# Kernel optimization log

Hardware: AMD Instinct MI355X
Metric: run time of the kernel (lower is better)

## Reference

```python
import jax, jax.numpy as jnp
import numpy as np

N, E, IN_DIM, OUT_DIM, NNZ = 4096, 2048, 256, 256, 65536
ALPHA = 0.2          # LeakyReLU negative slope
NEG_GAT = -9e15      # masked_fill value for GAT adjacency mask
NEG_ATT = -1e9       # masked_fill value inside ScaledDotProductAttention_hyper


def setup_inputs() -> dict:
    key = jax.random.key(0)
    ks = jax.random.split(key, 10)
    stdv = 1.0 / np.sqrt(OUT_DIM)
    u = lambda k, shape: jax.random.uniform(k, shape, jnp.float32, -stdv, stdv)
    x = jax.random.normal(ks[0], (N, IN_DIM), jnp.float32)
    node_idx = jax.random.randint(ks[1], (NNZ,), 0, N, jnp.int32)
    edge_idx = jax.random.randint(ks[2], (NNZ,), 0, E, jnp.int32)
    hyperedge_index = jnp.stack([node_idx, edge_idx])  # [2, NNZ]
    return {
        "x": x,
        "weight": u(ks[3], (IN_DIM, OUT_DIM)),
        "weight2": u(ks[4], (IN_DIM, OUT_DIM)),
        "weight3": u(ks[5], (OUT_DIM, OUT_DIM)),
        "weight_g": u(ks[6], (IN_DIM, OUT_DIM)),
        "a_g": u(ks[7], (2 * OUT_DIM, 1)),
        "word_context": u(ks[8], (1, OUT_DIM)),
        "bias": u(ks[9], (OUT_DIM,)),
        "hyperedge_index": hyperedge_index,
        "num_edges": E,
    }


def reference(x, weight, weight2, weight3, weight_g, a_g, word_context, bias,
              hyperedge_index, num_edges):
    n = x.shape[0]
    d = weight_g.shape[1]
    temp = d ** 0.5  # temperature = out_features ** 0.5

    # --- hypergraph preprocessing: dense incidence H [N, E] and node adjacency A [N, N]
    H = jnp.zeros((n, num_edges), x.dtype).at[hyperedge_index[0], hyperedge_index[1]].set(1.0)
    A = (H @ H.T > 0).astype(x.dtype)
    A = A.at[jnp.arange(n), jnp.arange(n)].set(1.0)  # fill_diagonal_(1)

    # --- dense GAT-style attention over the clique-expanded graph
    Wh_g = x @ weight_g                               # [N, D]
    Wh1 = Wh_g @ a_g[:d]                              # [N, 1]
    Wh2 = Wh_g @ a_g[d:]                              # [N, 1]
    e_g = jax.nn.leaky_relu(Wh1 + Wh2.T, ALPHA)       # [N, N]
    attention_g = jax.nn.softmax(jnp.where(A > 0, e_g, NEG_GAT), axis=1)

    # --- project node-node attention onto hyperedges: [N, E]
    graph2hyper = attention_g @ H

    # --- dual hypergraph cross-attention (eval mode: dropout is identity)
    x_4att = x @ weight2                              # [N, D]
    xw = x @ weight + bias                            # [N, D] (transfer=True)

    # attention1: hyperedge queries attend over nodes, mask = H.T [E, N]
    q1 = jnp.broadcast_to(word_context[0], (num_edges, d))
    attn1 = (q1 / temp) @ x_4att.T                    # [E, N]
    attn1 = jnp.where(H.T == 0, NEG_ATT, attn1)
    att1 = jax.nn.softmax(graph2hyper.T, axis=-1) + jax.nn.softmax(attn1, axis=-1)
    edge = att1 @ xw                                  # [E, D]
    att2he = att1.T                                   # [N, E]

    # attention2: node queries attend over hyperedges, mask = H [N, E]
    edge_4att = edge @ weight3                        # [E, D]
    attn2 = (x_4att / temp) @ edge_4att.T             # [N, E]
    attn2 = jnp.where(H == 0, NEG_ATT, attn2)
    att2hn = jax.nn.softmax(graph2hyper, axis=-1) + jax.nn.softmax(attn2, axis=-1)
    node = att2hn @ edge                              # [N, D]

    # --- combine attentions and aggregate
    att2_he_out = att2he @ att2he.T                   # [N, N]
    att2_hn_out = att2hn @ att2hn.T                   # [N, N]
    attention_out = attention_g + att2_he_out + att2_hn_out
    h_prime_g = jax.nn.elu(attention_out @ Wh_g)      # concat=True -> ELU

    node = jax.nn.relu(node)                          # concat=True -> ReLU, then squeeze
    return node, h_prime_g
```

## Files before the change

kernel.cpp:

```cpp
#include <hip/hip_runtime.h>
#include <cstdint>
#include <cstddef>


#define DI __device__ __forceinline__
typedef unsigned short u16;
typedef unsigned int   u32;
typedef __bf16 bf16x8 __attribute__((ext_vector_type(8)));
typedef float  f32x4  __attribute__((ext_vector_type(4)));
typedef u32    u32x4  __attribute__((ext_vector_type(4)));

constexpr int NN  = 4096;
constexpr int EE  = 2048;
constexpr int NNZb = 65536;

constexpr size_t MB = (size_t)1 << 20;
constexpr size_t OFF_HBITS   = 0;
constexpr size_t OFF_HBITST  = 1*MB;
constexpr size_t OFF_ABITS   = 2*MB;
constexpr size_t OFF_EDGE    = 2*MB;
constexpr size_t OFF_WH1     = 4*MB;
constexpr size_t OFF_WH2     = 4*MB + 16384;
constexpr size_t OFF_V       = 4*MB + 32768;
constexpr size_t OFF_RSINV   = 4*MB + 49152;
constexpr size_t OFF_WCAT    = 5*MB;
constexpr size_t OFF_XB      = 6*MB;
constexpr size_t OFF_EDGET   = 6*MB;
constexpr size_t OFF_HN2T    = 7*MB;
constexpr size_t OFF_WHG     = 8*MB;
constexpr size_t OFF_X4ATT   = 10*MB;
constexpr size_t OFF_YB      = 12*MB;
constexpr size_t OFF_XWT     = 14*MB;
constexpr size_t OFF_WHGTA   = 16*MB;
constexpr size_t OFF_HBT     = 18*MB;
constexpr size_t OFF_EDGE2T  = 18*MB;
constexpr size_t OFF_WHGTB   = 34*MB;
constexpr size_t OFF_EXPA    = 36*MB;
constexpr size_t OFF_ATT1    = 36*MB;
constexpr size_t OFF_ATT2HN  = 36*MB;
constexpr size_t OFF_ATT1T   = 52*MB;
constexpr size_t OFF_G2H     = 68*MB;
constexpr size_t OFF_G2HT    = 84*MB;
constexpr size_t OFF_ATT2HNT = 84*MB;
constexpr size_t OFF_ATTN2   = 100*MB;
constexpr size_t OFF_G1      = 116*MB;
constexpr size_t OFF_C2      = 120*MB;
constexpr size_t OFF_HN2ACC  = 124*MB;

DI u16 to_bf(float f) {
  union { float f; u32 u; } x; x.f = f;
  u32 r = x.u + 0x7fffu + ((x.u >> 16) & 1u);
  return (u16)(r >> 16);
}
DI float from_bf(u16 h) { union { u32 u; float f; } x; x.u = (u32)h << 16; return x.f; }
DI void store_bf4(u16* p, float a, float b, float c, float d) {
  u32 lo = (u32)to_bf(a) | ((u32)to_bf(b) << 16);
  u32 hi = (u32)to_bf(c) | ((u32)to_bf(d) << 16);
  *(u32*)p = lo; *((u32*)p + 1) = hi;
}

DI float wredf(float v) {
  #pragma unroll
  for (int o = 32; o; o >>= 1) v += __shfl_down(v, o);
  return v;
}
DI int wredi(int v) {
  #pragma unroll
  for (int o = 32; o; o >>= 1) v += __shfl_down(v, o);
  return v;
}

typedef __attribute__((address_space(3))) void lds_void;
typedef __attribute__((address_space(1))) void glb_void;
DI void async_load16(const void* g, void* l) {
  __builtin_amdgcn_global_load_lds((glb_void*)(uintptr_t)g,
                                   (lds_void*)(u32)(uintptr_t)l, 16, 0, 0);
}

template <int BM, int BN, class Epi>
DI void gemm_body(const u16* __restrict__ A, const u16* __restrict__ B,
                  int nb, int K, int k0, int kLen, Epi epi, int tile,
                  u16* As, u16* Bs)
{
  constexpr int BK = 64;
  constexpr int WM = BM / 2, WN = BN / 2;
  constexpr int FM = WM / 16, FN = WN / 16;
  constexpr int AI = (BM * 8) / 256, BI = (BN * 8) / 256;

  const int tid = threadIdx.x;
  const int w = tid >> 6, l = tid & 63;
  const int bi = tile / nb, bj = tile - bi * nb;
  const int i0 = bi * BM, j0 = bj * BN;
  const int wm = (w & 1) * WM, wn = (w >> 1) * WN;
  const int quad = l >> 4, m16 = l & 15;

  f32x4 acc[FM][FN] = {};

  for (int kb = k0; kb < k0 + kLen; kb += BK) {
    __syncthreads();
    #pragma unroll
    for (int i = 0; i < AI; ++i) {
      const int ci = (i * 4 + w) * 64 + l;
      const int r = ci >> 3;
      const int lc = (ci & 7) ^ (r & 7);
      async_load16(A + (size_t)(i0 + r) * K + kb + lc * 8, &As[(i * 4 + w) * 512]);
    }
    #pragma unroll
    for (int i = 0; i < BI; ++i) {
      const int ci = (i * 4 + w) * 64 + l;
      const int r = ci >> 3;
      const int lc = (ci & 7) ^ (r & 7);
      async_load16(B + (size_t)(j0 + r) * K + kb + lc * 8, &Bs[(i * 4 + w) * 512]);
    }
    __syncthreads();
    #pragma unroll
    for (int ks = 0; ks < 2; ++ks) {
      bf16x8 af[FM], bfv[FN];
      #pragma unroll
      for (int mi = 0; mi < FM; ++mi) {
        const int row = wm + mi * 16 + m16;
        af[mi] = *(const bf16x8*)&As[row * BK + (((ks * 4 + quad) ^ (row & 7)) * 8)];
      }
      #pragma unroll
      for (int ni = 0; ni < FN; ++ni) {
        const int row = wn + ni * 16 + m16;
        bfv[ni] = *(const bf16x8*)&Bs[row * BK + (((ks * 4 + quad) ^ (row & 7)) * 8)];
      }
      #pragma unroll
      for (int mi = 0; mi < FM; ++mi)
        #pragma unroll
        for (int ni = 0; ni < FN; ++ni)
          acc[mi][ni] = __builtin_amdgcn_mfma_f32_16x16x32_bf16(
              af[mi], bfv[ni], acc[mi][ni], 0, 0, 0);
    }
  }
  #pragma unroll
  for (int mi = 0; mi < FM; ++mi)
    #pragma unroll
    for (int ni = 0; ni < FN; ++ni) {
      const int rb = i0 + wm + mi * 16 + quad * 4;
      const int c  = j0 + wn + ni * 16 + m16;
      epi(rb, c, acc[mi][ni]);
    }
}

DI void t32_tile(const u16* __restrict__ in, u16* __restrict__ out,
                 int R, int C, int bx, int by, u16* t) {
  int tx = threadIdx.x & 31, ty = threadIdx.x >> 5;
  int x0 = bx * 32, y0 = by * 32;
  #pragma unroll
  for (int k = 0; k < 32; k += 8)
    t[(ty + k) * 33 + tx] = in[(size_t)(y0 + ty + k) * C + x0 + tx];
  __syncthreads();
  #pragma unroll
  for (int k = 0; k < 32; k += 8)
    out[(size_t)(x0 + ty + k) * R + y0 + tx] = t[tx * 33 + ty + k];
}

struct EpiG0 {
  u16 *whg, *whgTa, *whgTb, *x4, *xwT; const float* bias;
  DI void operator()(int r, int c, f32x4 v) const {
    if (c < 256) {
      #pragma unroll
      for (int i = 0; i < 4; ++i) whg[(r + i) * 256 + c] = to_bf(v[i]);
      store_bf4(&whgTa[(size_t)c * NN + r], v[0], v[1], v[2], v[3]);
      store_bf4(&whgTb[(size_t)c * NN + r], v[0], v[1], v[2], v[3]);
    } else if (c < 512) {
      #pragma unroll
      for (int i = 0; i < 4; ++i) x4[(r + i) * 256 + (c - 256)] = to_bf(v[i]);
    } else {
      float b = bias[c - 512];
      store_bf4(&xwT[(size_t)(c - 512) * NN + r], v[0]+b, v[1]+b, v[2]+b, v[3]+b);
    }
  }
};
struct EpiBig {
  const float* rsInv; u16* g2h; u16* g2hT; float* g1;
  DI void operator()(int r, int c, f32x4 v) const {
    float w0 = v[0]*rsInv[r], w1 = v[1]*rsInv[r+1], w2 = v[2]*rsInv[r+2], w3 = v[3]*rsInv[r+3];
    if (c < 2048) {
      g2h[(size_t)r * EE + c] = to_bf(w0);
      g2h[(size_t)(r+1) * EE + c] = to_bf(w1);
      g2h[(size_t)(r+2) * EE + c] = to_bf(w2);
      g2h[(size_t)(r+3) * EE + c] = to_bf(w3);
      store_bf4(&g2hT[(size_t)c * NN + r], w0, w1, w2, w3);
    } else {
      g1[(r) * 256 + (c - 2048)] = w0;
      g1[(r+1) * 256 + (c - 2048)] = w1;
      g1[(r+2) * 256 + (c - 2048)] = w2;
      g1[(r+3) * 256 + (c - 2048)] = w3;
    }
  }
};
struct EpiEdgeT {
  u16 *edgeT, *edge2T, *edge;
  DI void operator()(int r, int c, f32x4 v) const {
    if (r < 256) {
      #pragma unroll
      for (int i = 0; i < 4; ++i) edgeT[(size_t)(r + i) * EE + c] = to_bf(v[i]);
      store_bf4(&edge[(size_t)c * 256 + r], v[0], v[1], v[2], v[3]);
    } else {
      #pragma unroll
      for (int i = 0; i < 4; ++i) edge2T[(size_t)(r - 256 + i) * EE + c] = to_bf(v[i]);
    }
  }
};
struct EpiCombine {
  const float* g1; const float* c2; float* out;
  DI void operator()(int r, int c, f32x4 v) const {
    if (c < 256) {
      #pragma unroll
      for (int i = 0; i < 4; ++i) out[(r + i) * 256 + c] = fmaxf(v[i], 0.f);
    } else {
      int d = c - 256;
      #pragma unroll
      for (int i = 0; i < 4; ++i) {
        float s = g1[(r + i) * 256 + d] + c2[(r + i) * 256 + d] + v[i];
        out[1048576 + (r + i) * 256 + d] = s > 0.f ? s : expm1f(s);
      }
    }
  }
};
struct EpiBf16 { u16* out; int ldn;
  DI void operator()(int r, int c, f32x4 v) const {
    #pragma unroll
    for (int i = 0; i < 4; ++i) out[(size_t)(r + i) * ldn + c] = to_bf(v[i]);
  } };
struct EpiBf16Scale { u16* out; int ldn; float s;
  DI void operator()(int r, int c, f32x4 v) const {
    #pragma unroll
    for (int i = 0; i < 4; ++i) out[(size_t)(r + i) * ldn + c] = to_bf(v[i] * s);
  } };
struct EpiF32 { float* out; int ldn;
  DI void operator()(int r, int c, f32x4 v) const {
    #pragma unroll
    for (int i = 0; i < 4; ++i) out[(size_t)(r + i) * ldn + c] = v[i];
  } };
struct EpiAtomF32 { float* out; int ldn;
  DI void operator()(int r, int c, f32x4 v) const {
    #pragma unroll
    for (int i = 0; i < 4; ++i) atomicAdd(&out[(size_t)(r + i) * ldn + c], v[i]);
  } };

template <int BM, int BN, int S, int LB, int XSW, class Epi>
__global__ __launch_bounds__(256, LB)
void gemm_k(const u16* __restrict__ A, const u16* __restrict__ B,
            int nb, int K, Epi epi) {
  __shared__ __align__(16) u16 smem[(BM + BN) * 64];
  int t = blockIdx.x;
  int k0 = 0, kLen = K;
  if (XSW > 0) {
    const int xcd = t & 7, idx = t >> 3;
    const int bj = xcd * XSW + idx % XSW;
    const int bi = idx / XSW;
    t = bi * nb + bj;
  } else if (S > 1) {
    const int tilesPer = gridDim.x / S;
    const int s = t / tilesPer; t -= s * tilesPer;
    kLen = K / S; k0 = s * kLen;
  }
  gemm_body<BM, BN>(A, B, nb, K, k0, kLen, epi, t, smem, smem + BM * 64);
}

__global__ void k_prep(const float* wg, const float* w2, const float* w1,
                       const float* w3, const float* x, u16* wcat, u16* xb,
                       char* zbits, char* zhbt, char* zhn2) {
  int idx = blockIdx.x * 256 + threadIdx.x;
  if (blockIdx.x < 5120) {
    if (idx < 196608) {
      int blk = idx >> 16, r = idx & 65535;
      int d = r >> 8, kk = r & 255;
      const float* src = blk == 0 ? wg : blk == 1 ? w2 : w1;
      wcat[idx] = to_bf(src[kk * 256 + d]);
    } else if (idx < 262144) {
      int r = idx - 196608;
      wcat[196608 + r] = to_bf(w3[r]);
    } else {
      int r = idx - 262144;
      xb[r] = to_bf(x[r]);
    }
  } else {
    int z = idx - 5120 * 256;
    u32x4 zero = {0, 0, 0, 0};
    if (z < 262144)       ((u32x4*)zbits)[z] = zero;
    else if (z < 1310720) ((u32x4*)zhbt)[z - 262144] = zero;
    else                  ((u32x4*)zhn2)[z - 1310720] = zero;
  }
}

__global__ void k_scatter_diag(const int* __restrict__ hidx, u32* hbits, u32* hbitsT,
                               u16* hbT, u32* abits) {
  int k = blockIdx.x * 256 + threadIdx.x;
  if (k < NNZb) {
    int n = hidx[k], e = hidx[NNZb + k];
    atomicOr(&hbits[n * 64 + (e >> 5)], 1u << (e & 31));
    atomicOr(&hbitsT[e * 128 + (n >> 5)], 1u << (n & 31));
    hbT[(size_t)e * NN + n] = 0x3F80;
  } else {
    int i = k - NNZb;
    if (i < NN) atomicOr(&abits[i * 128 + (i >> 5)], 1u << (i & 31));
  }
}

__global__ void k_rowclique(const u16* __restrict__ whg, const u16* __restrict__ x4,
                            const float* __restrict__ ag, const float* __restrict__ wc,
                            float* wh1, float* wh2, float* v,
                            const u32* __restrict__ hbitsT, u32* abits) {
  __shared__ int list[512];
  __shared__ int cnt;
  int tid = threadIdx.x;
  if (blockIdx.x < 1024) {
    int wv = tid >> 6, l = tid & 63;
    int row = blockIdx.x * 4 + wv;
    float s1 = 0, s2 = 0, s3 = 0;
    #pragma unroll
    for (int dd = 0; dd < 4; ++dd) {
      int d = l * 4 + dd;
      float a = from_bf(whg[row * 256 + d]);
      s1 += a * ag[d]; s2 += a * ag[256 + d];
      s3 += from_bf(x4[row * 256 + d]) * wc[d];
    }
    s1 = wredf(s1); s2 = wredf(s2); s3 = wredf(s3);
    if (l == 0) { wh1[row] = s1; wh2[row] = s2; v[row] = s3 * (1.0f / 16.0f); }
  } else {
    int e = blockIdx.x - 1024;
    if (tid == 0) cnt = 0;
    __syncthreads();
    if (tid < 128) {
      u32 w = hbitsT[e * 128 + tid];
      while (w) {
        int b = __ffs(w) - 1;
        int p = atomicAdd(&cnt, 1);
        if (p < 512) list[p] = tid * 32 + b;
        w &= w - 1;
      }
    }
    __syncthreads();
    int c = cnt < 512 ? cnt : 512;
    for (int p = tid; p < c * c; p += 256) {
      int i = list[p / c], j = list[p % c];
      atomicOr(&abits[i * 128 + (j >> 5)], 1u << (j & 31));
    }
  }
}

__global__ void k_exprows(const u32* __restrict__ abits, const float* __restrict__ wh1,
                          const float* __restrict__ wh2, u16* __restrict__ expA,
                          float* rsInv) {
  int i = blockIdx.x, tid = threadIdx.x;
  __shared__ float w2s[NN];
  __shared__ float ssum;
  for (int j = tid; j < NN; j += 256) w2s[j] = wh2[j];
  if (tid == 0) ssum = 0.f;
  __syncthreads();
  float a = wh1[i], lsum = 0.f;
  for (int j = tid; j < NN; j += 256) {
    u32 w = abits[i * 128 + (j >> 5)];
    u16 h = 0;
    if ((w >> (j & 31)) & 1) {
      float z = a + w2s[j];
      float eg = z > 0.f ? z : 0.2f * z;
      h = to_bf(__expf(eg));
      lsum += from_bf(h);
    }
    expA[(size_t)i * NN + j] = h;
  }
  lsum = wredf(lsum);
  if ((tid & 63) == 0) atomicAdd(&ssum, lsum);
  __syncthreads();
  if (tid == 0) rsInv[i] = 1.0f / ssum;
}

__global__ void k_edge_softmax(const u16* __restrict__ g2hT, const u32* __restrict__ hbitsT,
                               const float* __restrict__ v, u16* __restrict__ att1) {
  int e = blockIdx.x, tid = threadIdx.x;
  __shared__ float evals[NN];
  __shared__ u32 hw[128];
  __shared__ float s1s, s2s; __shared__ int cs;
  if (tid == 0) { s1s = 0.f; s2s = 0.f; cs = 0; }
  if (tid < 128) hw[tid] = hbitsT[e * 128 + tid];
  __syncthreads();
  float sum1 = 0.f;
  for (int j = tid; j < NN; j += 256) {
    float ev = __expf(from_bf(g2hT[(size_t)e * NN + j]));
    evals[j] = ev; sum1 += ev;
  }
  float sum2 = 0.f; int cnt = 0;
  if (tid < 128) {
    u32 w = hw[tid]; cnt = __popc(w);
    while (w) { int b = __ffs(w) - 1; sum2 += __expf(v[tid * 32 + b]); w &= w - 1; }
  }
  sum1 = wredf(sum1); sum2 = wredf(sum2); cnt = wredi(cnt);
  if ((tid & 63) == 0) { atomicAdd(&s1s, sum1); atomicAdd(&s2s, sum2); atomicAdd(&cs, cnt); }
  __syncthreads();
  float inv1 = 1.0f / s1s;
  int c = cs;
  float inv2 = c > 0 ? 1.0f / s2s : 0.0f;
  float unif = c > 0 ? 0.0f : (1.0f / (float)NN);
  for (int j = tid; j < NN; j += 256) {
    float t = evals[j] * inv1 + unif;
    if ((hw[j >> 5] >> (j & 31)) & 1) t += __expf(v[j]) * inv2;
    att1[(size_t)e * NN + j] = to_bf(t);
  }
}

__global__ __launch_bounds__(256, 2)
void k_tri_edge(const u16* __restrict__ Fcat, const u16* __restrict__ Att1,
                EpiEdgeT e0,
                const u16* __restrict__ X4att, const u16* __restrict__ W3b,
                EpiBf16 e1,
                const u16* __restrict__ tin, u16* __restrict__ tout) {
  __shared__ __align__(16) u16 smem[192 * 64];
  int b = blockIdx.x;
  if (b < 256) {
    const int xcd = b & 7, idx = b >> 3;
    const int t = (idx / 4) * 32 + xcd * 4 + (idx & 3);
    gemm_body<64, 64>(Fcat, Att1, 32, NN, 0, NN, e0, t, smem, smem + 64 * 64);
  }
  else if (b < 384) gemm_body<128, 64>(X4att, W3b, 4, 256, 0, 256, e1, b - 256, smem, smem + 128 * 64);
  else { int t = b - 384; t32_tile(tin, tout, EE, NN, t & 127, t >> 7, smem); }
}

__global__ __launch_bounds__(256, 2)
void k_dual_attn2(const u16* __restrict__ Att1T, const u16* __restrict__ Edge2T,
                  EpiF32 e0,
                  const u16* __restrict__ Yb, const u16* __restrict__ Edge,
                  EpiBf16Scale e1) {
  __shared__ __align__(16) u16 smem[256 * 64];
  int b = blockIdx.x;
  if (b < 128) gemm_body<128, 64>(Att1T, Edge2T, 4, EE, 0, EE, e0, b, smem, smem + 128 * 64);
  else         gemm_body<128, 128>(Yb, Edge, 16, 256, 0, 256, e1, b - 128, smem, smem + 128 * 64);
}

__global__ void k_node_softmax(const u16* __restrict__ g2h, const u16* __restrict__ attn2,
                               const u32* __restrict__ hbits, u16* __restrict__ att2hn) {
  int n = blockIdx.x, tid = threadIdx.x;
  __shared__ float ev3[EE], ev4[EE];
  __shared__ u32 hw[64];
  __shared__ float s3s, s4s; __shared__ int cs;
  if (tid == 0) { s3s = 0.f; s4s = 0.f; cs = 0; }
  if (tid < 64) hw[tid] = hbits[n * 64 + tid];
  __syncthreads();
  float s3 = 0.f, s4 = 0.f; int cl = 0;
  for (int e = tid; e < EE; e += 256) {
    float x3 = __expf(from_bf(g2h[(size_t)n * EE + e]));
    ev3[e] = x3; s3 += x3;
    bool m = (hw[e >> 5] >> (e & 31)) & 1;
    float x4 = m ? __expf(from_bf(attn2[(size_t)n * EE + e])) : 0.f;
    ev4[e] = x4; s4 += x4; cl += m;
  }
  s3 = wredf(s3); s4 = wredf(s4); cl = wredi(cl);
  if ((tid & 63) == 0) { atomicAdd(&s3s, s3); atomicAdd(&s4s, s4); atomicAdd(&cs, cl); }
  __syncthreads();
  float inv3 = 1.0f / s3s;
  int c = cs;
  float inv4 = c > 0 ? 1.0f / s4s : 0.0f;
  float unif = c > 0 ? 0.0f : (1.0f / (float)EE);
  for (int e = tid; e < EE; e += 256)
    att2hn[(size_t)n * EE + e] = to_bf(ev3[e] * inv3 + ev4[e] * inv4 + unif);
}

__global__ void k_transpose(const u16* __restrict__ in, u16* __restrict__ out,
                            int R, int C) {
  __shared__ u16 t[32 * 33];
  t32_tile(in, out, R, C, blockIdx.x, blockIdx.y, t);
}

__global__ void k_cast_hn2(const float* __restrict__ acc, u16* __restrict__ hn2T) {
  int idx = blockIdx.x * 256 + threadIdx.x;
  hn2T[idx] = to_bf(acc[idx]);
}

extern "C" void kernel_launch(void* const* d_in, const int* in_sizes, int n_in,
                              void* d_out, int out_size, void* d_ws, size_t ws_size,
                              hipStream_t stream) {
  (void)in_sizes; (void)n_in; (void)out_size; (void)ws_size;
  const float* x    = (const float*)d_in[0];
  const float* w1   = (const float*)d_in[1];
  const float* w2   = (const float*)d_in[2];
  const float* w3   = (const float*)d_in[3];
  const float* wg   = (const float*)d_in[4];
  const float* ag   = (const float*)d_in[5];
  const float* wc   = (const float*)d_in[6];
  const float* bias = (const float*)d_in[7];
  const int*   hidx = (const int*)d_in[8];
  float* out = (float*)d_out;
  char* ws = (char*)d_ws;

  u32* Hbits   = (u32*)(ws + OFF_HBITS);
  u32* HbitsT  = (u32*)(ws + OFF_HBITST);
  u32* Abits   = (u32*)(ws + OFF_ABITS);
  float* Wh1   = (float*)(ws + OFF_WH1);
  float* Wh2   = (float*)(ws + OFF_WH2);
  float* V     = (float*)(ws + OFF_V);
  float* RsInv = (float*)(ws + OFF_RSINV);
  u16* Wcat    = (u16*)(ws + OFF_WCAT);
  u16* W3b     = Wcat + 196608;
  u16* Xb      = (u16*)(ws + OFF_XB);
  u16* Whg     = (u16*)(ws + OFF_WHG);
  u16* X4att   = (u16*)(ws + OFF_X4ATT);
  u16* Yb      = (u16*)(ws + OFF_YB);
  u16* XwT     = (u16*)(ws + OFF_XWT);
  u16* WhgTa   = (u16*)(ws + OFF_WHGTA);
  u16* HbT     = (u16*)(ws + OFF_HBT);
  u16* WhgTb   = (u16*)(ws + OFF_WHGTB);
  u16* ExpA    = (u16*)(ws + OFF_EXPA);
  u16* Att1    = (u16*)(ws + OFF_ATT1);
  u16* Att1T   = (u16*)(ws + OFF_ATT1T);
  u16* Att2hn  = (u16*)(ws + OFF_ATT2HN);
  u16* G2h     = (u16*)(ws + OFF_G2H);
  u16* G2hT    = (u16*)(ws + OFF_G2HT);
  u16* Att2hnT = (u16*)(ws + OFF_ATT2HNT);
  u16* Attn2   = (u16*)(ws + OFF_ATTN2);
  float* G1    = (float*)(ws + OFF_G1);
  float* C2    = (float*)(ws + OFF_C2);
  float* Hn2Acc = (float*)(ws + OFF_HN2ACC);
  u16* Edge    = (u16*)(ws + OFF_EDGE);
  u16* EdgeT   = (u16*)(ws + OFF_EDGET);
  u16* Hn2T    = (u16*)(ws + OFF_HN2T);
  u16* Edge2T  = (u16*)(ws + OFF_EDGE2T);

  k_prep<<<10752, 256, 0, stream>>>(wg, w2, w1, w3, x, Wcat, Xb,
                                    ws + OFF_HBITS, ws + OFF_HBT, ws + OFF_HN2ACC);
  k_scatter_diag<<<272, 256, 0, stream>>>(hidx, Hbits, HbitsT, HbT, Abits);
  gemm_k<128, 64, 1, 3, 0><<<384, 256, 0, stream>>>(
      Xb, Wcat, 12, 256, EpiG0{Whg, WhgTa, WhgTb, X4att, XwT, bias});
  k_rowclique<<<3072, 256, 0, stream>>>(Whg, X4att, ag, wc, Wh1, Wh2, V,
                                        HbitsT, Abits);
  k_exprows<<<NN, 256, 0, stream>>>(Abits, Wh1, Wh2, ExpA, RsInv);
  gemm_k<128, 96, 1, 3, 3><<<768, 256, 0, stream>>>(
      ExpA, HbT, 24, NN, EpiBig{RsInv, G2h, G2hT, G1});
  k_edge_softmax<<<EE, 256, 0, stream>>>(G2hT, HbitsT, V, Att1);
  k_tri_edge<<<8576, 256, 0, stream>>>(
      XwT, Att1, EpiEdgeT{EdgeT, Edge2T, Edge},
      X4att, W3b, EpiBf16{Yb, 256},
      Att1, Att1T);
  k_dual_attn2<<<640, 256, 0, stream>>>(
      Att1T, Edge2T, EpiF32{C2, 256},
      Yb, Edge, EpiBf16Scale{Attn2, EE, 1.0f / 16.0f});
  k_node_softmax<<<NN, 256, 0, stream>>>(G2h, Attn2, Hbits, Att2hn);
  k_transpose<<<dim3(64, 128), 256, 0, stream>>>(Att2hn, Att2hnT, NN, EE);
  gemm_k<64, 64, 4, 3, 0><<<512, 256, 0, stream>>>(
      WhgTa, Att2hnT, 32, NN, EpiAtomF32{Hn2Acc, EE});
  k_cast_hn2<<<2048, 256, 0, stream>>>(Hn2Acc, Hn2T);
  gemm_k<64, 64, 1, 2, 0><<<512, 256, 0, stream>>>(
      Att2hn, EdgeT, 8, EE, EpiCombine{G1, C2, out});
}
```

Before: 380.3 us.

## Run the big exp(A) x [H|Whg] GEMM in FP8 with a dedicated kernel

The large N x N by N x (E+D) GEMM now takes fp8 (e4m3) operands. expA, the incidence matrix H^T and the second transposed copy of Wh_g are stored as fp8, and a new gemm_f8 kernel with swizzled LDS tiles and 16x16x32 fp8 MFMA replaces the bf16 GEMM. This halves the bytes read from memory and the LDS traffic, and doubles MFMA throughput for the largest matmul. In exchange, exp values and Wh_g lose precision, and the XCD tile swizzle of the old GEMM is dropped.

New measurement: 361.4 us. 5.0% less time.

```diff
diff --git a/kernel.cpp b/kernel.cpp
--- a/kernel.cpp
+++ b/kernel.cpp
@@ -5,6 +5,7 @@
 
 #define DI __device__ __forceinline__
 typedef unsigned short u16;
+typedef unsigned char  u8;
 typedef unsigned int   u32;
 typedef __bf16 bf16x8 __attribute__((ext_vector_type(8)));
 typedef float  f32x4  __attribute__((ext_vector_type(4)));
@@ -34,7 +35,7 @@
 constexpr size_t OFF_WHGTA   = 16*MB;
 constexpr size_t OFF_HBT     = 18*MB;
 constexpr size_t OFF_EDGE2T  = 18*MB;
-constexpr size_t OFF_WHGTB   = 34*MB;
+constexpr size_t OFF_WHGTB   = 26*MB;
 constexpr size_t OFF_EXPA    = 36*MB;
 constexpr size_t OFF_ATT1    = 36*MB;
 constexpr size_t OFF_ATT2HN  = 36*MB;
@@ -58,6 +59,11 @@
   u32 hi = (u32)to_bf(c) | ((u32)to_bf(d) << 16);
   *(u32*)p = lo; *((u32*)p + 1) = hi;
 }
+DI u32 pack_fp8x4(float a, float b, float c, float d) {
+  int p = __builtin_amdgcn_cvt_pk_fp8_f32(a, b, 0, false);
+  p = __builtin_amdgcn_cvt_pk_fp8_f32(c, d, p, true);
+  return (u32)p;
+}
 
 DI float wredf(float v) {
   #pragma unroll
@@ -158,13 +164,13 @@
 }
 
 struct EpiG0 {
-  u16 *whg, *whgTa, *whgTb, *x4, *xwT; const float* bias;
+  u16 *whg, *whgTa, *x4, *xwT; u8* whgTb; const float* bias;
   DI void operator()(int r, int c, f32x4 v) const {
     if (c < 256) {
       #pragma unroll
       for (int i = 0; i < 4; ++i) whg[(r + i) * 256 + c] = to_bf(v[i]);
       store_bf4(&whgTa[(size_t)c * NN + r], v[0], v[1], v[2], v[3]);
-      store_bf4(&whgTb[(size_t)c * NN + r], v[0], v[1], v[2], v[3]);
+      *(u32*)&whgTb[(size_t)c * NN + r] = pack_fp8x4(v[0], v[1], v[2], v[3]);
     } else if (c < 512) {
       #pragma unroll
       for (int i = 0; i < 4; ++i) x4[(r + i) * 256 + (c - 256)] = to_bf(v[i]);
@@ -242,24 +248,88 @@
     for (int i = 0; i < 4; ++i) atomicAdd(&out[(size_t)(r + i) * ldn + c], v[i]);
   } };
 
-template <int BM, int BN, int S, int LB, int XSW, class Epi>
+template <int BM, int BN, int S, int LB, class Epi>
 __global__ __launch_bounds__(256, LB)
 void gemm_k(const u16* __restrict__ A, const u16* __restrict__ B,
             int nb, int K, Epi epi) {
   __shared__ __align__(16) u16 smem[(BM + BN) * 64];
   int t = blockIdx.x;
   int k0 = 0, kLen = K;
-  if (XSW > 0) {
-    const int xcd = t & 7, idx = t >> 3;
-    const int bj = xcd * XSW + idx % XSW;
-    const int bi = idx / XSW;
-    t = bi * nb + bj;
-  } else if (S > 1) {
+  if (S > 1) {
     const int tilesPer = gridDim.x / S;
     const int s = t / tilesPer; t -= s * tilesPer;
     kLen = K / S; k0 = s * kLen;
   }
   gemm_body<BM, BN>(A, B, nb, K, k0, kLen, epi, t, smem, smem + BM * 64);
+}
+
+template <class Epi>
+__global__ __launch_bounds__(256, 3)
+void gemm_f8(const u8* __restrict__ A, const u8* __restrict__ B,
+             int nb, int K, Epi epi) {
+  constexpr int BM = 128, BN = 96, BK = 128;
+  constexpr int FM = 4, FN = 3;
+  __shared__ __align__(16) u8 As[BM * BK];
+  __shared__ __align__(16) u8 Bs[BN * BK];
+
+  const int tid = threadIdx.x;
+  const int w = tid >> 6, l = tid & 63;
+  const int tile = blockIdx.x;
+  const int bi = tile / nb, bj = tile - bi * nb;
+  const int i0 = bi * BM, j0 = bj * BN;
+  const int wm = (w & 1) * 64, wn = (w >> 1) * 48;
+  const int quad = l >> 4, m16 = l & 15;
+
+  f32x4 acc[FM][FN] = {};
+
+  for (int kb = 0; kb < K; kb += BK) {
+    __syncthreads();
+    #pragma unroll
+    for (int i = 0; i < 4; ++i) {
+      const int ci = (i * 4 + w) * 64 + l;
+      const int r = ci >> 3;
+      const int lc = (ci & 7) ^ (r & 7);
+      async_load16(A + (size_t)(i0 + r) * K + kb + lc * 16, &As[(i * 4 + w) * 1024]);
+    }
+    #pragma unroll
+    for (int i = 0; i < 3; ++i) {
+      const int ci = (i * 4 + w) * 64 + l;
+      const int r = ci >> 3;
+      const int lc = (ci & 7) ^ (r & 7);
+      async_load16(B + (size_t)(j0 + r) * K + kb + lc * 16, &Bs[(i * 4 + w) * 1024]);
+    }
+    __syncthreads();
+    #pragma unroll
+    for (int ks = 0; ks < 4; ++ks) {
+      const int lcl = ks * 2 + (quad >> 1);
+      const int sub = (quad & 1) * 8;
+      long af[FM], bf[FN];
+      #pragma unroll
+      for (int mi = 0; mi < FM; ++mi) {
+        const int row = wm + mi * 16 + m16;
+        af[mi] = *(const long*)&As[row * BK + (lcl ^ (row & 7)) * 16 + sub];
+      }
+      #pragma unroll
+      for (int ni = 0; ni < FN; ++ni) {
+        const int row = wn + ni * 16 + m16;
+        bf[ni] = *(const long*)&Bs[row * BK + (lcl ^ (row & 7)) * 16 + sub];
+      }
+      #pragma unroll
+      for (int mi = 0; mi < FM; ++mi)
+        #pragma unroll
+        for (int ni = 0; ni < FN; ++ni)
+          acc[mi][ni] = __builtin_amdgcn_mfma_f32_16x16x32_fp8_fp8(
+              af[mi], bf[ni], acc[mi][ni], 0, 0, 0);
+    }
+  }
+  #pragma unroll
+  for (int mi = 0; mi < FM; ++mi)
+    #pragma unroll
+    for (int ni = 0; ni < FN; ++ni) {
+      const int rb = i0 + wm + mi * 16 + quad * 4;
+      const int c  = j0 + wn + ni * 16 + m16;
+      epi(rb, c, acc[mi][ni]);
+    }
 }
 
 __global__ void k_prep(const float* wg, const float* w2, const float* w1,
@@ -282,20 +352,20 @@
   } else {
     int z = idx - 5120 * 256;
     u32x4 zero = {0, 0, 0, 0};
-    if (z < 262144)       ((u32x4*)zbits)[z] = zero;
-    else if (z < 1310720) ((u32x4*)zhbt)[z - 262144] = zero;
-    else                  ((u32x4*)zhn2)[z - 1310720] = zero;
+    if (z < 262144)      ((u32x4*)zbits)[z] = zero;
+    else if (z < 786432) ((u32x4*)zhbt)[z - 262144] = zero;
+    else                 ((u32x4*)zhn2)[z - 786432] = zero;
   }
 }
 
 __global__ void k_scatter_diag(const int* __restrict__ hidx, u32* hbits, u32* hbitsT,
-                               u16* hbT, u32* abits) {
+                               u8* hbT, u32* abits) {
   int k = blockIdx.x * 256 + threadIdx.x;
   if (k < NNZb) {
     int n = hidx[k], e = hidx[NNZb + k];
     atomicOr(&hbits[n * 64 + (e >> 5)], 1u << (e & 31));
     atomicOr(&hbitsT[e * 128 + (n >> 5)], 1u << (n & 31));
-    hbT[(size_t)e * NN + n] = 0x3F80;
+    hbT[(size_t)e * NN + n] = 0x38;
   } else {
     int i = k - NNZb;
     if (i < NN) atomicOr(&abits[i * 128 + (i >> 5)], 1u << (i & 31));
@@ -345,7 +415,7 @@
 }
 
 __global__ void k_exprows(const u32* __restrict__ abits, const float* __restrict__ wh1,
-                          const float* __restrict__ wh2, u16* __restrict__ expA,
+                          const float* __restrict__ wh2, u8* __restrict__ expA,
                           float* rsInv) {
   int i = blockIdx.x, tid = threadIdx.x;
   __shared__ float w2s[NN];
@@ -354,16 +424,20 @@
   if (tid == 0) ssum = 0.f;
   __syncthreads();
   float a = wh1[i], lsum = 0.f;
-  for (int j = tid; j < NN; j += 256) {
+  #pragma unroll
+  for (int it = 0; it < 4; ++it) {
+    int j = it * 1024 + tid * 4;
     u32 w = abits[i * 128 + (j >> 5)];
-    u16 h = 0;
-    if ((w >> (j & 31)) & 1) {
-      float z = a + w2s[j];
-      float eg = z > 0.f ? z : 0.2f * z;
-      h = to_bf(__expf(eg));
-      lsum += from_bf(h);
-    }
-    expA[(size_t)i * NN + j] = h;
+    u32 m = (w >> (j & 31)) & 0xFu;
+    float x0 = 0.f, x1 = 0.f, x2 = 0.f, x3 = 0.f;
+    if (m & 1u) { float z = a + w2s[j];     float eg = z > 0.f ? z : 0.2f * z; x0 = __expf(eg); }
+    if (m & 2u) { float z = a + w2s[j + 1]; float eg = z > 0.f ? z : 0.2f * z; x1 = __expf(eg); }
+    if (m & 4u) { float z = a + w2s[j + 2]; float eg = z > 0.f ? z : 0.2f * z; x2 = __expf(eg); }
+    if (m & 8u) { float z = a + w2s[j + 3]; float eg = z > 0.f ? z : 0.2f * z; x3 = __expf(eg); }
+    u32 word = pack_fp8x4(x0, x1, x2, x3);
+    *(u32*)&expA[(size_t)i * NN + j] = word;
+    lsum += __builtin_amdgcn_cvt_f32_fp8(word, 0) + __builtin_amdgcn_cvt_f32_fp8(word, 1)
+          + __builtin_amdgcn_cvt_f32_fp8(word, 2) + __builtin_amdgcn_cvt_f32_fp8(word, 3);
   }
   lsum = wredf(lsum);
   if ((tid & 63) == 0) atomicAdd(&ssum, lsum);
@@ -502,9 +576,9 @@
   u16* Yb      = (u16*)(ws + OFF_YB);
   u16* XwT     = (u16*)(ws + OFF_XWT);
   u16* WhgTa   = (u16*)(ws + OFF_WHGTA);
-  u16* HbT     = (u16*)(ws + OFF_HBT);
-  u16* WhgTb   = (u16*)(ws + OFF_WHGTB);
-  u16* ExpA    = (u16*)(ws + OFF_EXPA);
+  u8*  HbT8    = (u8*)(ws + OFF_HBT);
+  u8*  WhgTb8  = (u8*)(ws + OFF_WHGTB);
+  u8*  ExpA8   = (u8*)(ws + OFF_EXPA);
   u16* Att1    = (u16*)(ws + OFF_ATT1);
   u16* Att1T   = (u16*)(ws + OFF_ATT1T);
   u16* Att2hn  = (u16*)(ws + OFF_ATT2HN);
@@ -520,16 +594,16 @@
   u16* Hn2T    = (u16*)(ws + OFF_HN2T);
   u16* Edge2T  = (u16*)(ws + OFF_EDGE2T);
 
-  k_prep<<<10752, 256, 0, stream>>>(wg, w2, w1, w3, x, Wcat, Xb,
-                                    ws + OFF_HBITS, ws + OFF_HBT, ws + OFF_HN2ACC);
-  k_scatter_diag<<<272, 256, 0, stream>>>(hidx, Hbits, HbitsT, HbT, Abits);
-  gemm_k<128, 64, 1, 3, 0><<<384, 256, 0, stream>>>(
-      Xb, Wcat, 12, 256, EpiG0{Whg, WhgTa, WhgTb, X4att, XwT, bias});
+  k_prep<<<8704, 256, 0, stream>>>(wg, w2, w1, w3, x, Wcat, Xb,
+                                   ws + OFF_HBITS, ws + OFF_HBT, ws + OFF_HN2ACC);
+  k_scatter_diag<<<272, 256, 0, stream>>>(hidx, Hbits, HbitsT, HbT8, Abits);
+  gemm_k<128, 64, 1, 3><<<384, 256, 0, stream>>>(
+      Xb, Wcat, 12, 256, EpiG0{Whg, WhgTa, X4att, XwT, WhgTb8, bias});
   k_rowclique<<<3072, 256, 0, stream>>>(Whg, X4att, ag, wc, Wh1, Wh2, V,
                                         HbitsT, Abits);
-  k_exprows<<<NN, 256, 0, stream>>>(Abits, Wh1, Wh2, ExpA, RsInv);
-  gemm_k<128, 96, 1, 3, 3><<<768, 256, 0, stream>>>(
-      ExpA, HbT, 24, NN, EpiBig{RsInv, G2h, G2hT, G1});
+  k_exprows<<<NN, 256, 0, stream>>>(Abits, Wh1, Wh2, ExpA8, RsInv);
+  gemm_f8<<<768, 256, 0, stream>>>(
+      ExpA8, HbT8, 24, NN, EpiBig{RsInv, G2h, G2hT, G1});
   k_edge_softmax<<<EE, 256, 0, stream>>>(G2hT, HbitsT, V, Att1);
   k_tri_edge<<<8576, 256, 0, stream>>>(
       XwT, Att1, EpiEdgeT{EdgeT, Edge2T, Edge},
@@ -540,9 +614,9 @@
       Yb, Edge, EpiBf16Scale{Attn2, EE, 1.0f / 16.0f});
   k_node_softmax<<<NN, 256, 0, stream>>>(G2h, Attn2, Hbits, Att2hn);
   k_transpose<<<dim3(64, 128), 256, 0, stream>>>(Att2hn, Att2hnT, NN, EE);
-  gemm_k<64, 64, 4, 3, 0><<<512, 256, 0, stream>>>(
+  gemm_k<64, 64, 4, 3><<<512, 256, 0, stream>>>(
       WhgTa, Att2hnT, 32, NN, EpiAtomF32{Hn2Acc, EE});
   k_cast_hn2<<<2048, 256, 0, stream>>>(Hn2Acc, Hn2T);
-  gemm_k<64, 64, 1, 2, 0><<<512, 256, 0, stream>>>(
+  gemm_k<64, 64, 1, 2><<<512, 256, 0, stream>>>(
       Att2hn, EdgeT, 8, EE, EpiCombine{G1, C2, out});
 }
```
